# Kernel optimization log

Hardware: AMD Instinct MI355X
Metric: run time of the kernel (lower is better)

## Reference

```python
import jax, jax.numpy as jnp
import numpy as np

NUM_DIRECTIONS = 64
NUM_STEPS = 64
D = 64
NEG_INF = -1e9  # matches the original's -inf sentinel of 1e9


def _sample_directions(n):
    # Mirrors WeightedEulerCurve._obtainDirection with np.random.seed(4)
    np.random.seed(4)
    out = []
    for _ in range(n):
        phi = np.random.uniform(0, np.pi * 2)
        costheta = np.random.uniform(-1, 1)
        theta = np.arccos(costheta)
        out.append([np.sin(theta) * np.cos(phi), np.sin(theta) * np.sin(phi), np.cos(theta)])
    return np.asarray(out, dtype=np.float32)


def setup_inputs() -> dict:
    key = jax.random.key(0)
    # strictly positive -> dense cubical complex (every voxel is a vertex,
    # every adjacent pair an edge, etc.), matching torch.nonzero on x>0
    x = jax.random.uniform(key, (D, D, D), dtype=jnp.float32) + 1e-3
    dirs = jnp.asarray(_sample_directions(NUM_DIRECTIONS))  # (K, 3)
    return {"x": x, "dirs": dirs}


def _pairmax(a, axis):
    n = a.shape[axis]
    return jnp.maximum(jax.lax.slice_in_dim(a, 0, n - 1, axis=axis),
                       jax.lax.slice_in_dim(a, 1, n, axis=axis))


def _curve_contrib(heights, vals, intervals):
    # heights: (K, N) per-direction simplex heights; vals: (N,) shared weights
    K = heights.shape[0]
    idx = jnp.argsort(heights, axis=-1)
    sorted_h = jnp.take_along_axis(heights, idx, axis=-1)
    sorted_v = jnp.take(vals, idx)                                    # (K, N)
    csum = jnp.concatenate([jnp.zeros((K, 1), heights.dtype),
                            jnp.cumsum(sorted_v, axis=-1)], axis=-1)  # (K, N+1)
    padded_h = jnp.concatenate([jnp.full((K, 1), NEG_INF, heights.dtype),
                                sorted_h], axis=-1)                   # (K, N+1)
    ptr = jax.vmap(lambda h: jnp.searchsorted(h, intervals, side='right'))(padded_h) - 1
    return jnp.take_along_axis(csum, ptr, axis=-1)                    # (K, num_intervals)


def _wect(x, dirs, num_steps):
    d = x.shape[0]
    K = dirs.shape[0]
    r = jnp.arange(d, dtype=x.dtype)
    d0, d1, d2 = dirs[:, 0], dirs[:, 1], dirs[:, 2]
    # vertex heights per direction: H[k,i,j,l] = d0*i + d1*j + d2*l
    H = (d0[:, None, None, None] * r[:, None, None]
         + d1[:, None, None, None] * r[None, :, None]
         + d2[:, None, None, None] * r[None, None, :])
    p0, p1, p2 = (jax.nn.relu(d0)[:, None], jax.nn.relu(d1)[:, None], jax.nn.relu(d2)[:, None])

    min_h = -(3.0 ** 0.5) * d
    dh = (-2.0 * min_h) / num_steps
    intervals = jnp.asarray(min_h + dh * np.arange(num_steps + 1), dtype=x.dtype)

    # vertices
    vh = H.reshape(K, -1)
    vv = x.reshape(-1)

    # edges along each axis: max over the 2 endpoints -> base height + relu(d_axis)
    eh = jnp.concatenate([
        H[:, :-1].reshape(K, -1) + p0,
        H[:, :, :-1].reshape(K, -1) + p1,
        H[:, :, :, :-1].reshape(K, -1) + p2], axis=1)
    ev = jnp.concatenate([
        _pairmax(x, 0).reshape(-1),
        _pairmax(x, 1).reshape(-1),
        _pairmax(x, 2).reshape(-1)])

    # squares spanning axis pairs (1,2), (0,2), (0,1): max over 4 corners
    sh = jnp.concatenate([
        H[:, :, :-1, :-1].reshape(K, -1) + p1 + p2,
        H[:, :-1, :, :-1].reshape(K, -1) + p0 + p2,
        H[:, :-1, :-1, :].reshape(K, -1) + p0 + p1], axis=1)
    sv = jnp.concatenate([
        _pairmax(_pairmax(x, 1), 2).reshape(-1),
        _pairmax(_pairmax(x, 0), 2).reshape(-1),
        _pairmax(_pairmax(x, 0), 1).reshape(-1)])

    # cubes: max over 8 corners
    ch = H[:, :-1, :-1, :-1].reshape(K, -1) + p0 + p1 + p2
    cv = _pairmax(_pairmax(_pairmax(x, 0), 1), 2).reshape(-1)

    v = _curve_contrib(vh, vv, intervals)
    e = _curve_contrib(eh, ev, intervals)
    s = _curve_contrib(sh, sv, intervals)
    c = _curve_contrib(ch, cv, intervals)
    return v - e + s - c  # (K, num_steps + 1)


def reference(x, dirs):
    return _wect(x, dirs, NUM_STEPS)
```

## Files before the change

kernel.cpp:

```cpp
#include <hip/hip_runtime.h>
#include <math.h>

#define NDIRS 64
#define NBIN 65
#define HIST1 4224
#define STAGEF 512
#define THREADS 256
#define WPB 4
#define SPW 2
#define NBLK 512
#define ROWF (NDIRS*NBIN)
#define MROWS 64

static constexpr float INV = 0.28867513459481287f;

__global__ __launch_bounds__(THREADS) void wect_hist(
    const float* __restrict__ x, const float* __restrict__ dirs,
    float* __restrict__ accum) {
  __shared__ float hist[WPB * HIST1];
  __shared__ float stage[WPB * STAGEF];
  const int tid = threadIdx.x;
  const int lane = tid & 63;
  const int wid  = tid >> 6;

  float4* h4 = (float4*)hist;
  for (int idx = tid; idx < WPB * HIST1 / 4; idx += THREADS)
    h4[idx] = make_float4(0.f, 0.f, 0.f, 0.f);
  __syncthreads();

  const float D0 = dirs[3*lane+0] * INV;
  const float D1 = dirs[3*lane+1] * INV;
  const float D2 = dirs[3*lane+2] * INV;
  const float Q1 = fmaxf(D0, 0.f);
  const float Q2 = fmaxf(D1, 0.f);
  const float Q3 = fmaxf(D2, 0.f);
  const float Q4 = Q2 + Q3;
  const float Q5 = Q1 + Q3;
  const float Q6 = Q1 + Q2;
  const float Q7 = Q1 + Q2 + Q3;

  float* __restrict__ myh = hist + wid * HIST1 + lane;
  float4* __restrict__ mystage = (float4*)(stage + wid * STAGEF);

  for (int s = 0; s < SPW; ++s) {
    const int strip = (blockIdx.x * WPB + wid) * SPW + s;
    const int i = strip >> 6, j = strip & 63;
    const int l = lane;
    const float* p = x + (strip << 6) + l;
    const int dL = (l < 63) ? 1 : 0;
    const int dJ = (j < 63) ? 64 : 0;
    const int dI = (i < 63) ? 4096 : 0;
    const bool iv = dI != 0, jv = dJ != 0, lv = dL != 0;

    const float x000 = p[0],       x001 = p[dL];
    const float x010 = p[dJ],      x011 = p[dJ+dL];
    const float x100 = p[dI],      x101 = p[dI+dL];
    const float x110 = p[dI+dJ],   x111 = p[dI+dJ+dL];

    const float e0m = fmaxf(x000, x100);
    const float e1m = fmaxf(x000, x010);
    const float e2m = fmaxf(x000, x001);
    const float s12 = fmaxf(fmaxf(e1m, x001), x011);
    const float s02 = fmaxf(fmaxf(e0m, x001), x101);
    const float s01 = fmaxf(fmaxf(e0m, x010), x110);
    const float cc  = fmaxf(fmaxf(s01, fmaxf(x001, x101)), fmaxf(x011, x111));

    const float v1 = iv ? -e0m : 0.f;
    const float v2 = jv ? -e1m : 0.f;
    const float v3 = lv ? -e2m : 0.f;
    const float v4 = (jv && lv) ? s12 : 0.f;
    const float v5 = (iv && lv) ? s02 : 0.f;
    const float v6 = (iv && jv) ? s01 : 0.f;
    const float v7 = (iv && jv && lv) ? -cc : 0.f;
    const float T  = x000 + v1+v2+v3+v4+v5+v6+v7;

    mystage[2*lane]     = make_float4(T,  v1, v2, v3);
    mystage[2*lane + 1] = make_float4(v4, v5, v6, v7);

    const float u0 = (float)i * D0 + (float)j * D1;

    #pragma unroll 8
    for (int t = 0; t < 64; ++t) {
      const float4 A = mystage[2*t];
      const float4 B = mystage[2*t + 1];
      const float u  = fmaf((float)t, D2, u0);
      const float bf = ceilf(u);
      const float fr = bf - u;
      const int   ib = (int)bf + 32;
      float S = 0.f;
      S += (Q1 > fr) ? A.y : 0.f;
      S += (Q2 > fr) ? A.z : 0.f;
      S += (Q3 > fr) ? A.w : 0.f;
      S += (Q4 > fr) ? B.x : 0.f;
      S += (Q5 > fr) ? B.y : 0.f;
      S += (Q6 > fr) ? B.z : 0.f;
      S += (Q7 > fr) ? B.w : 0.f;
      float* a = myh + (ib << 6);
      const float r0 = a[0], r1 = a[64];
      a[0]  = r0 + (A.x - S);
      a[64] = r1 + S;
    }
  }

  __syncthreads();
  float* __restrict__ obase = accum + blockIdx.x * ROWF;
  for (int z = tid; z < ROWF; z += THREADS)
    obase[z] = hist[z] + hist[HIST1 + z]
             + hist[2*HIST1 + z] + hist[3*HIST1 + z];
}

__global__ __launch_bounds__(256) void wect_reduceA(
    const float* __restrict__ accum, float* __restrict__ mid) {
  const int q = blockIdx.x * 256 + threadIdx.x;
  if (q >= MROWS * ROWF) return;
  const int g = q / ROWF, z = q - g * ROWF;
  float v = 0.f;
  #pragma unroll
  for (int m = 0; m < NBLK / MROWS; ++m)
    v += accum[(g * (NBLK / MROWS) + m) * ROWF + z];
  mid[g * ROWF + z] = v;
}

__global__ __launch_bounds__(512) void wect_scan(
    const float* __restrict__ mid, float* __restrict__ out) {
  __shared__ float red[8 * NBIN];
  __shared__ float s[NBIN];
  const int k = blockIdx.x, tid = threadIdx.x;
  for (int z = tid; z < 8 * NBIN; z += 512) {
    const int g = z / NBIN, c = z - g * NBIN;
    float v = 0.f;
    #pragma unroll
    for (int r = g; r < MROWS; r += 8) v += mid[r * ROWF + (c << 6) + k];
    red[z] = v;
  }
  __syncthreads();
  if (tid < NBIN) {
    float v = 0.f;
    #pragma unroll
    for (int gg = 0; gg < 8; ++gg) v += red[gg * NBIN + tid];
    s[tid] = v;
  }
  __syncthreads();
  for (int off = 1; off < NBIN; off <<= 1) {
    float a = 0.f;
    if (tid < NBIN && tid >= off) a = s[tid - off];
    __syncthreads();
    if (tid < NBIN && tid >= off) s[tid] += a;
    __syncthreads();
  }
  if (tid < NBIN) out[k * NBIN + tid] = s[tid];
}

extern "C" void kernel_launch(void* const* d_in, const int* in_sizes, int n_in,
                              void* d_out, int out_size, void* d_ws, size_t ws_size,
                              hipStream_t stream) {
  const float* x = (const float*)d_in[0];
  const float* dirs = (const float*)d_in[1];
  float* out = (float*)d_out;
  float* accum = (float*)d_ws;
  float* mid = accum + NBLK * ROWF;

  wect_hist<<<NBLK, THREADS, 0, stream>>>(x, dirs, accum);
  wect_reduceA<<<(MROWS * ROWF + 255) / 256, 256, 0, stream>>>(accum, mid);
  wect_scan<<<NDIRS, 512, 0, stream>>>(mid, out);
}
```

Before: 83.85 us.

## Use per-strip sliding-window histograms to shrink LDS and run 8 waves per block

Each wave's histogram now covers only the bins its strip can reach along the lane axis (a 21-bin window starting at the minimum ceil of the height), instead of all 65 bins. The smaller LDS footprint lets a block hold 8 waves of 512 threads, each handling one strip, instead of 4 waves with two strips each. The final reduction remaps each wave's window back to absolute bins using the stored per-direction base offsets. The aim is higher occupancy and less LDS zeroing and reduction traffic. In exchange, the window width is a fixed assumption: it must hold the bin span plus the +1 neighbour write, and the reduction gains bounds checks.

New measurement: 85.06 us. About the same (+1.4%).

```diff
diff --git a/kernel.cpp b/kernel.cpp
--- a/kernel.cpp
+++ b/kernel.cpp
@@ -3,11 +3,11 @@
 
 #define NDIRS 64
 #define NBIN 65
-#define HIST1 4224
+#define WIN 21
+#define WROW (WIN*64)
 #define STAGEF 512
-#define THREADS 256
-#define WPB 4
-#define SPW 2
+#define THREADS 512
+#define WPB 8
 #define NBLK 512
 #define ROWF (NDIRS*NBIN)
 #define MROWS 64
@@ -17,14 +17,15 @@
 __global__ __launch_bounds__(THREADS) void wect_hist(
     const float* __restrict__ x, const float* __restrict__ dirs,
     float* __restrict__ accum) {
-  __shared__ float hist[WPB * HIST1];
+  __shared__ float histw[WPB * WROW];
   __shared__ float stage[WPB * STAGEF];
+  __shared__ int   b0s[WPB * 64];
   const int tid = threadIdx.x;
   const int lane = tid & 63;
   const int wid  = tid >> 6;
 
-  float4* h4 = (float4*)hist;
-  for (int idx = tid; idx < WPB * HIST1 / 4; idx += THREADS)
+  float4* h4 = (float4*)histw;
+  for (int idx = tid; idx < WPB * WROW / 4; idx += THREADS)
     h4[idx] = make_float4(0.f, 0.f, 0.f, 0.f);
   __syncthreads();
 
@@ -39,11 +40,11 @@
   const float Q6 = Q1 + Q2;
   const float Q7 = Q1 + Q2 + Q3;
 
-  float* __restrict__ myh = hist + wid * HIST1 + lane;
+  float* __restrict__ myhw = histw + wid * WROW + lane;
   float4* __restrict__ mystage = (float4*)(stage + wid * STAGEF);
 
-  for (int s = 0; s < SPW; ++s) {
-    const int strip = (blockIdx.x * WPB + wid) * SPW + s;
+  {
+    const int strip = blockIdx.x * WPB + wid;
     const int i = strip >> 6, j = strip & 63;
     const int l = lane;
     const float* p = x + (strip << 6) + l;
@@ -79,6 +80,12 @@
 
     const float u0 = (float)i * D0 + (float)j * D1;
 
+    const float u63 = fmaf(63.f, D2, u0);
+    const int ib0  = (int)ceilf(u0);
+    const int ib63 = (int)ceilf(u63);
+    const int wbase = min(ib0, ib63);
+    b0s[wid*64 + lane] = wbase + 32;
+
     #pragma unroll 8
     for (int t = 0; t < 64; ++t) {
       const float4 A = mystage[2*t];
@@ -86,7 +93,7 @@
       const float u  = fmaf((float)t, D2, u0);
       const float bf = ceilf(u);
       const float fr = bf - u;
-      const int   ib = (int)bf + 32;
+      const int   w  = (int)bf - wbase;
       float S = 0.f;
       S += (Q1 > fr) ? A.y : 0.f;
       S += (Q2 > fr) ? A.z : 0.f;
@@ -95,7 +102,7 @@
       S += (Q5 > fr) ? B.y : 0.f;
       S += (Q6 > fr) ? B.z : 0.f;
       S += (Q7 > fr) ? B.w : 0.f;
-      float* a = myh + (ib << 6);
+      float* a = myhw + (w << 6);
       const float r0 = a[0], r1 = a[64];
       a[0]  = r0 + (A.x - S);
       a[64] = r1 + S;
@@ -104,9 +111,25 @@
 
   __syncthreads();
   float* __restrict__ obase = accum + blockIdx.x * ROWF;
-  for (int z = tid; z < ROWF; z += THREADS)
-    obase[z] = hist[z] + hist[HIST1 + z]
-             + hist[2*HIST1 + z] + hist[3*HIST1 + z];
+  const int k = tid & 63;
+  const int b0 = b0s[0*64 + k], b1 = b0s[1*64 + k],
+            b2 = b0s[2*64 + k], b3 = b0s[3*64 + k],
+            b4 = b0s[4*64 + k], b5 = b0s[5*64 + k],
+            b6 = b0s[6*64 + k], b7 = b0s[7*64 + k];
+  for (int z = tid; z < ROWF; z += THREADS) {
+    const int c = z >> 6;
+    float v = 0.f;
+    int w;
+    w = c - b0; if ((unsigned)w < WIN) v += histw[0*WROW + (w << 6) + k];
+    w = c - b1; if ((unsigned)w < WIN) v += histw[1*WROW + (w << 6) + k];
+    w = c - b2; if ((unsigned)w < WIN) v += histw[2*WROW + (w << 6) + k];
+    w = c - b3; if ((unsigned)w < WIN) v += histw[3*WROW + (w << 6) + k];
+    w = c - b4; if ((unsigned)w < WIN) v += histw[4*WROW + (w << 6) + k];
+    w = c - b5; if ((unsigned)w < WIN) v += histw[5*WROW + (w << 6) + k];
+    w = c - b6; if ((unsigned)w < WIN) v += histw[6*WROW + (w << 6) + k];
+    w = c - b7; if ((unsigned)w < WIN) v += histw[7*WROW + (w << 6) + k];
+    obase[z] = v;
+  }
 }
 
 __global__ __launch_bounds__(256) void wect_reduceA(
```
